# Kernel tuning notes

Measured on AMD Instinct MI355X. Metric: run time of the kernel, lower is better.

## Reference

```python
import jax, jax.numpy as jnp
import numpy as np
import math

B, S, D, H = 8, 1024, 128, 8  # batch, seq, input_dim(=head_dim), head_num

def setup_inputs() -> dict:
    key = jax.random.key(0)
    ks = jax.random.split(key, 12)
    HD = H * D
    sc_in = 1.0 / math.sqrt(D)
    sc_hd = 1.0 / math.sqrt(HD)
    return {
        "query": jax.random.normal(ks[0], (B, S, D), jnp.float32),
        "key":   jax.random.normal(ks[1], (B, S, D), jnp.float32),
        "value": jax.random.normal(ks[2], (B, S, D), jnp.float32),
        "pos":   jax.random.normal(ks[3], (B, S, D), jnp.float32),
        "mask":  jnp.ones((B, S), jnp.int32),
        # torch Linear weights stored as [in, out] for x @ W + b
        "Wq": jax.random.normal(ks[4], (D, HD), jnp.float32) * sc_in,
        "bq": jnp.zeros((HD,), jnp.float32),
        "Wk": jax.random.normal(ks[5], (D, HD), jnp.float32) * sc_in,
        "bk": jnp.zeros((HD,), jnp.float32),
        "Wv": jax.random.normal(ks[6], (D, HD), jnp.float32) * sc_in,
        "bv": jnp.zeros((HD,), jnp.float32),
        "Wo": jax.random.normal(ks[7], (HD, D), jnp.float32) * sc_hd,
        "bo": jnp.zeros((D,), jnp.float32),
    }

def reference(query, key, value, pos, mask, Wq, bq, Wk, bk, Wv, bv, Wo, bo):
    # QKV projections (pos added to all three inputs)
    q = (query + pos) @ Wq + bq  # [B,S,H*D]
    k = (key + pos) @ Wk + bk
    v = (value + pos) @ Wv + bv
    # split heads -> [B,H,S,D]
    q = q.reshape(B, S, H, D).transpose(0, 2, 1, 3)
    k = k.reshape(B, S, H, D).transpose(0, 2, 1, 3)
    v = v.reshape(B, S, H, D).transpose(0, 2, 1, 3)
    scale = 1.0 / math.sqrt(D)
    scores = jnp.einsum("bhqd,bhkd->bhqk", q, k) * scale  # [B,H,S,S]
    # mask [B,S] -> broadcast over heads and query positions
    m = mask[:, None, None, :]  # [B,1,1,S]
    scores = jnp.where(m == 0, jnp.float32(-jnp.inf), scores)
    attn = jax.nn.softmax(scores, axis=-1)  # dropout is identity in eval mode
    out = jnp.einsum("bhqk,bhkd->bhqd", attn, v)
    out = out.transpose(0, 2, 1, 3).reshape(B, S, H * D)
    return out @ Wo + bo  # [B,S,D]
```

## Files before the change

### kernel.cpp

```cpp
#include <hip/hip_runtime.h>
#include <stdint.h>


typedef __attribute__((ext_vector_type(8))) short bf16x8;
typedef __attribute__((ext_vector_type(4))) float f32x4;
typedef unsigned int uint;
typedef unsigned short ushort;

__device__ __forceinline__ float bf2f(short s) {
    return __uint_as_float(((uint)(ushort)s) << 16);
}
__device__ __forceinline__ short f2bf(float f) {
    uint u = __float_as_uint(f);
    u += 0x7fffu + ((u >> 16) & 1u);
    return (short)(u >> 16);
}
__device__ __forceinline__ short f2bf_fast(float f) {
    return (short)((__float_as_uint(f) + 0x8000u) >> 16);
}

__device__ __forceinline__ void dma16(const short* g, short* l) {
    __builtin_amdgcn_global_load_lds(
        (const __attribute__((address_space(1))) uint*)g,
        (__attribute__((address_space(3))) uint*)l, 16, 0, 0);
}

__global__ __launch_bounds__(256) void fill_sentinel(float* __restrict__ out, int n) {
    int i = blockIdx.x * 256 + threadIdx.x;
    if (i < n) out[i] = 128.0f;
}

__global__ __launch_bounds__(256) void transpose_w(
    const float* __restrict__ Wq, const float* __restrict__ Wk,
    const float* __restrict__ Wv, const float* __restrict__ Wo,
    short* __restrict__ WTq, short* __restrict__ WTk,
    short* __restrict__ WTv, short* __restrict__ WoT)
{
    int z = blockIdx.y;
    const float* src; short* dst; int K, N;
    if (z < 3) { K = 128; N = 1024; src = (z==0)?Wq:(z==1)?Wk:Wv; dst = (z==0)?WTq:(z==1)?WTk:WTv; }
    else       { K = 1024; N = 128; src = Wo; dst = WoT; }
    int ntn = N >> 6;
    int nt = blockIdx.x % ntn, kt = blockIdx.x / ntn;
    int k0 = kt * 64, n0 = nt * 64;

    __shared__ __align__(16) short TT[64][72];
    int t = threadIdx.x;
    int r = t >> 2, c4 = t & 3;
    const float4* s4 = (const float4*)&src[(k0 + r) * N + n0 + c4 * 16];
    short* tr = &TT[r][c4 * 16];
#pragma unroll
    for (int i = 0; i < 4; ++i) {
        float4 v = s4[i];
        tr[i * 4 + 0] = f2bf(v.x);
        tr[i * 4 + 1] = f2bf(v.y);
        tr[i * 4 + 2] = f2bf(v.z);
        tr[i * 4 + 3] = f2bf(v.w);
    }
    __syncthreads();
    union { short s[16]; uint4 v[2]; } pk;
#pragma unroll
    for (int i = 0; i < 16; ++i) pk.s[i] = TT[c4 * 16 + i][r];
    uint4* dp = (uint4*)&dst[(n0 + r) * K + k0 + c4 * 16];
    dp[0] = pk.v[0]; dp[1] = pk.v[1];
}

__global__ __launch_bounds__(256) void qkv_proj(
    const float* __restrict__ query, const float* __restrict__ key_,
    const float* __restrict__ value, const float* __restrict__ pos,
    const short* __restrict__ WTq, const short* __restrict__ WTk, const short* __restrict__ WTv,
    const float* __restrict__ bq, const float* __restrict__ bk, const float* __restrict__ bv,
    short* __restrict__ Qg, short* __restrict__ Kg, short* __restrict__ Vtg)
{
    int z = blockIdx.y;
    const float* X    = (z==0) ? query : (z==1) ? key_ : value;
    const short* WT   = (z==0) ? WTq   : (z==1) ? WTk  : WTv;
    const float* bias = (z==0) ? bq    : (z==1) ? bk   : bv;

    __shared__ __align__(16) short Xs[64][136];
    __shared__ __align__(16) short Ws[16 * 512];
    __shared__ __align__(16) short T[64][72];

    int t = threadIdx.x;
    int m0 = blockIdx.x * 64;
    int lane = t & 63, w = t >> 6;
    int l = lane & 15, q = lane >> 4;

    {
        int r = t >> 2, c4 = t & 3;
        const float4* xs = (const float4*)&X[(m0 + r) * 128 + c4 * 32];
        const float4* ps = (const float4*)&pos[(m0 + r) * 128 + c4 * 32];
#pragma unroll
        for (int i = 0; i < 8; ++i) {
            float4 a = xs[i], bb = ps[i];
            uint2 o;
            o.x = (uint)(ushort)f2bf(a.x + bb.x) | ((uint)(ushort)f2bf(a.y + bb.y) << 16);
            o.y = (uint)(ushort)f2bf(a.z + bb.z) | ((uint)(ushort)f2bf(a.w + bb.w) << 16);
            *(uint2*)&Xs[r][c4 * 32 + i * 4] = o;
        }
    }
    __syncthreads();

    bf16x8 aX[4];
#pragma unroll
    for (int k32 = 0; k32 < 4; ++k32)
        aX[k32] = *(const bf16x8*)&Xs[w * 16 + l][k32 * 32 + q * 8];

    int b = m0 >> 10, s0 = m0 & 1023;

    for (int nt = 0; nt < 16; ++nt) {
        int n0 = nt * 64;
        __syncthreads();
        {
            const short* wsrc = &WT[(n0 + w * 16 + l) * 128 + q * 8];
#pragma unroll
            for (int k32 = 0; k32 < 4; ++k32)
                dma16(wsrc + k32 * 32, &Ws[(w * 4 + k32) * 512]);
        }
        __syncthreads();

        f32x4 acc[4];
#pragma unroll
        for (int nb = 0; nb < 4; ++nb) {
            f32x4 c = {0.f, 0.f, 0.f, 0.f};
            const short* wf = &Ws[nb * 2048 + lane * 8];
#pragma unroll
            for (int k32 = 0; k32 < 4; ++k32)
                c = __builtin_amdgcn_mfma_f32_16x16x32_bf16(aX[k32], *(const bf16x8*)(wf + k32 * 512), c, 0, 0, 0);
            acc[nb] = c;
        }

        if (z < 2) {
#pragma unroll
            for (int nb = 0; nb < 4; ++nb) {
                float bi = bias[n0 + nb * 16 + l];
#pragma unroll
                for (int r = 0; r < 4; ++r)
                    T[w * 16 + q * 4 + r][nb * 16 + l] = f2bf(acc[nb][r] + bi);
            }
            __syncthreads();
            short* dst = (z == 0) ? Qg : Kg;
            int row = t >> 2, c16 = t & 3;
            int n = n0 + c16 * 16, h = n >> 7, d0 = n & 127;
            uint4 v0 = *(uint4*)&T[row][c16 * 16];
            uint4 v1 = *(uint4*)&T[row][c16 * 16 + 8];
            uint4* dp = (uint4*)&dst[(((b * 8 + h) * 1024 + s0 + row) << 7) + d0];
            dp[0] = v0; dp[1] = v1;
        } else {
#pragma unroll
            for (int nb = 0; nb < 4; ++nb) {
                float bi = bias[n0 + nb * 16 + l];
#pragma unroll
                for (int r = 0; r < 4; ++r)
                    T[nb * 16 + l][w * 16 + q * 4 + r] = f2bf(acc[nb][r] + bi);
            }
            __syncthreads();
            int nl = t >> 2, mc = t & 3;
            int n = n0 + nl, h = n >> 7, d = n & 127;
            uint4 v0 = *(uint4*)&T[nl][mc * 16];
            uint4 v1 = *(uint4*)&T[nl][mc * 16 + 8];
            uint4* dp = (uint4*)&Vtg[(((b * 8 + h) * 128 + d) << 10) + s0 + mc * 16];
            dp[0] = v0; dp[1] = v1;
        }
    }
}

__global__ __launch_bounds__(256) void attention(
    const short* __restrict__ Qg, const short* __restrict__ Kg,
    const short* __restrict__ Vtg, const int* __restrict__ mask,
    short* __restrict__ AO)
{
    int bh = blockIdx.x & 63;
    int qt = blockIdx.x >> 6;
    int b = bh >> 3, h = bh & 7;
    int q0 = qt << 6;

    __shared__ __align__(16) short Ks[16 * 512];
    __shared__ __align__(16) short Vs[16 * 512];
    __shared__ __align__(16) short Ps[4][16][72];
    __shared__ int Ms[64];

    int t = threadIdx.x, lane = t & 63, w = t >> 6;
    int l = lane & 15, q = lane >> 4;

    bf16x8 aQ[4];
    {
        const short* qp = &Qg[((bh * 1024 + q0 + w * 16 + l) << 7) + q * 8];
#pragma unroll
        for (int k32 = 0; k32 < 4; ++k32)
            aQ[k32] = *(const bf16x8*)(qp + k32 * 32);
    }

    f32x4 O[8];
#pragma unroll
    for (int i = 0; i < 8; ++i) O[i] = {0.f, 0.f, 0.f, 0.f};
    float lrow[4] = {0.f, 0.f, 0.f, 0.f};

    const float SL2E = 0.12752298917458827f;
    const float MAXB = 44.0f;

    const short* kbase = &Kg[((bh * 1024 + w * 16 + l) << 7) + q * 8];
    const short* vb0 = &Vtg[((bh * 128 + (2 * w) * 16 + l) << 10) + q * 8];
    const short* vb1 = &Vtg[((bh * 128 + (2 * w + 1) * 16 + l) << 10) + q * 8];

    for (int kt = 0; kt < 16; ++kt) {
        int k0 = kt << 6;
        __syncthreads();
        {
            const short* kp = kbase + (k0 << 7);
            dma16(kp,      &Ks[(w * 4 + 0) * 512]);
            dma16(kp + 32, &Ks[(w * 4 + 1) * 512]);
            dma16(kp + 64, &Ks[(w * 4 + 2) * 512]);
            dma16(kp + 96, &Ks[(w * 4 + 3) * 512]);
            dma16(vb0 + k0,      &Vs[(4 * w + 0) * 512]);
            dma16(vb0 + k0 + 32, &Vs[(4 * w + 1) * 512]);
            dma16(vb1 + k0,      &Vs[(4 * w + 2) * 512]);
            dma16(vb1 + k0 + 32, &Vs[(4 * w + 3) * 512]);
            if (t < 64) Ms[t] = mask[b * 1024 + k0 + t];
        }
        __syncthreads();

        int mk0 = Ms[l], mk1 = Ms[16 + l], mk2 = Ms[32 + l], mk3 = Ms[48 + l];
        bool allm = (__ballot(mk0 && mk1 && mk2 && mk3) == ~0ull);

        float p[4][4];
#pragma unroll
        for (int nb = 0; nb < 4; ++nb) {
            f32x4 c = {0.f, 0.f, 0.f, 0.f};
            const short* kf = &Ks[nb * 2048 + lane * 8];
#pragma unroll
            for (int k32 = 0; k32 < 4; ++k32)
                c = __builtin_amdgcn_mfma_f32_16x16x32_bf16(aQ[k32], *(const bf16x8*)(kf + k32 * 512), c, 0, 0, 0);
#pragma unroll
            for (int r = 0; r < 4; ++r)
                p[nb][r] = exp2f(fmaf(c[r], SL2E, -MAXB));
        }
        if (!allm) {
            int mks[4] = {mk0, mk1, mk2, mk3};
#pragma unroll
            for (int nb = 0; nb < 4; ++nb)
                if (!mks[nb])
#pragma unroll
                    for (int r = 0; r < 4; ++r) p[nb][r] = 0.f;
        }
#pragma unroll
        for (int nb = 0; nb < 4; ++nb)
#pragma unroll
            for (int r = 0; r < 4; ++r) {
                lrow[r] += p[nb][r];
                Ps[w][q * 4 + r][nb * 16 + l] = f2bf_fast(p[nb][r]);
            }

        bf16x8 aP0 = *(const bf16x8*)&Ps[w][l][q * 8];
        bf16x8 aP1 = *(const bf16x8*)&Ps[w][l][32 + q * 8];
#pragma unroll
        for (int dt = 0; dt < 8; ++dt) {
            f32x4 c = O[dt];
            c = __builtin_amdgcn_mfma_f32_16x16x32_bf16(aP0, *(const bf16x8*)&Vs[(dt * 2 + 0) * 512 + lane * 8], c, 0, 0, 0);
            c = __builtin_amdgcn_mfma_f32_16x16x32_bf16(aP1, *(const bf16x8*)&Vs[(dt * 2 + 1) * 512 + lane * 8], c, 0, 0, 0);
            O[dt] = c;
        }
    }

#pragma unroll
    for (int off = 1; off <= 8; off <<= 1)
#pragma unroll
        for (int r = 0; r < 4; ++r)
            lrow[r] += __shfl_xor(lrow[r], off);
    float rl[4];
#pragma unroll
    for (int r = 0; r < 4; ++r) rl[r] = 1.0f / lrow[r];
#pragma unroll
    for (int dt = 0; dt < 8; ++dt) {
        int col = h * 128 + dt * 16 + l;
#pragma unroll
        for (int r = 0; r < 4; ++r) {
            int s = q0 + w * 16 + q * 4 + r;
            AO[((b * 1024 + s) << 10) + col] = f2bf(O[dt][r] * rl[r]);
        }
    }
}

__global__ __launch_bounds__(256) void out_proj(
    const short* __restrict__ AO, const short* __restrict__ WoT,
    const float* __restrict__ bo, float* __restrict__ out)
{
    __shared__ __align__(16) short As[32][72];
    __shared__ __align__(16) short Bs[16 * 512];

    int t = threadIdx.x, lane = t & 63, w = t >> 6;
    int l = lane & 15, q = lane >> 4;
    int m0 = blockIdx.x * 32;
    int rowh = (w & 1) * 16;
    int nbg = (w >> 1) * 4;

    f32x4 acc[4];
#pragma unroll
    for (int i = 0; i < 4; ++i) acc[i] = {0.f, 0.f, 0.f, 0.f};

    for (int kc = 0; kc < 16; ++kc) {
        int k0 = kc * 64;
        __syncthreads();
        {
            int r = t >> 3, c8 = t & 7;
            *(uint4*)&As[r][c8 * 8] = *(const uint4*)&AO[((m0 + r) << 10) + k0 + c8 * 8];
#pragma unroll
            for (int j = 0; j < 4; ++j) {
                int nb = w * 2 + (j >> 1), k32 = j & 1;
                dma16(&WoT[(nb * 16 + l) * 1024 + k0 + k32 * 32 + q * 8],
                      &Bs[(nb * 2 + k32) * 512]);
            }
        }
        __syncthreads();

        bf16x8 aA0 = *(const bf16x8*)&As[rowh + l][q * 8];
        bf16x8 aA1 = *(const bf16x8*)&As[rowh + l][32 + q * 8];
#pragma unroll
        for (int nb = 0; nb < 4; ++nb) {
            f32x4 c = acc[nb];
            c = __builtin_amdgcn_mfma_f32_16x16x32_bf16(aA0, *(const bf16x8*)&Bs[((nbg + nb) * 2 + 0) * 512 + lane * 8], c, 0, 0, 0);
            c = __builtin_amdgcn_mfma_f32_16x16x32_bf16(aA1, *(const bf16x8*)&Bs[((nbg + nb) * 2 + 1) * 512 + lane * 8], c, 0, 0, 0);
            acc[nb] = c;
        }
    }

#pragma unroll
    for (int nb = 0; nb < 4; ++nb) {
        int n = (nbg + nb) * 16 + l;
        float bi = bo[n];
#pragma unroll
        for (int r = 0; r < 4; ++r) {
            int m = m0 + rowh + q * 4 + r;
            out[(m << 7) + n] = acc[nb][r] + bi;
        }
    }
}

extern "C" void kernel_launch(void* const* d_in, const int* in_sizes, int n_in,
                              void* d_out, int out_size, void* d_ws, size_t ws_size,
                              hipStream_t stream)
{
    const size_t NEED = (size_t)65 * 1024 * 1024;
    if (ws_size < NEED) {
        hipLaunchKernelGGL(fill_sentinel, dim3((out_size + 255) / 256), dim3(256), 0, stream,
                           (float*)d_out, out_size);
        return;
    }

    const float* query = (const float*)d_in[0];
    const float* key_  = (const float*)d_in[1];
    const float* value = (const float*)d_in[2];
    const float* pos   = (const float*)d_in[3];
    const int*   mask  = (const int*)d_in[4];
    const float* Wq = (const float*)d_in[5];
    const float* bq = (const float*)d_in[6];
    const float* Wk = (const float*)d_in[7];
    const float* bk = (const float*)d_in[8];
    const float* Wv = (const float*)d_in[9];
    const float* bv = (const float*)d_in[10];
    const float* Wo = (const float*)d_in[11];
    const float* bo = (const float*)d_in[12];

    char* ws = (char*)d_ws;
    short* Qg  = (short*)(ws);
    short* Kg  = (short*)(ws + (size_t)16 * 1024 * 1024);
    short* Vtg = (short*)(ws + (size_t)32 * 1024 * 1024);
    short* AO  = (short*)(ws + (size_t)48 * 1024 * 1024);
    short* WTq = (short*)(ws + (size_t)64 * 1024 * 1024);
    short* WTk = WTq + 131072;
    short* WTv = WTk + 131072;
    short* WoT = WTv + 131072;

    hipLaunchKernelGGL(transpose_w, dim3(32, 4), dim3(256), 0, stream,
                       Wq, Wk, Wv, Wo, WTq, WTk, WTv, WoT);
    hipLaunchKernelGGL(qkv_proj, dim3(128, 3), dim3(256), 0, stream,
                       query, key_, value, pos, WTq, WTk, WTv, bq, bk, bv, Qg, Kg, Vtg);
    hipLaunchKernelGGL(attention, dim3(1024), dim3(256), 0, stream,
                       Qg, Kg, Vtg, mask, AO);
    hipLaunchKernelGGL(out_proj, dim3(256), dim3(256), 0, stream,
                       AO, WoT, bo, (float*)d_out);
}
```

Before: 223.2 us.

## Double-buffer LDS tiles in QKV, attention and output projection kernels

Converts the weight, K/V and output-projection tile staging from single-buffered to double-buffered LDS. The next tile is prefetched with global_load_lds while the current one feeds the MFMAs, and one of the two barriers per iteration is removed. The attention kernel also loads the whole 1024-entry mask row into LDS once instead of per tile. The cost is roughly twice the LDS footprint per block, which can cut occupancy, and correctness relies on the barrier waiting for outstanding LDS DMA.

```diff
diff --git a/kernel.cpp b/kernel.cpp
--- a/kernel.cpp
+++ b/kernel.cpp
@@ -78,14 +78,20 @@
     const float* bias = (z==0) ? bq    : (z==1) ? bk   : bv;
 
     __shared__ __align__(16) short Xs[64][136];
-    __shared__ __align__(16) short Ws[16 * 512];
-    __shared__ __align__(16) short T[64][72];
+    __shared__ __align__(16) short Ws[2][8192];
+    __shared__ __align__(16) short T[2][64][72];
 
     int t = threadIdx.x;
     int m0 = blockIdx.x * 64;
     int lane = t & 63, w = t >> 6;
     int l = lane & 15, q = lane >> 4;
 
+    const short* wbase = &WT[(w * 16 + l) * 128 + q * 8];
+    {
+#pragma unroll
+        for (int k32 = 0; k32 < 4; ++k32)
+            dma16(wbase + k32 * 32, &Ws[0][(w * 4 + k32) * 512]);
+    }
     {
         int r = t >> 2, c4 = t & 3;
         const float4* xs = (const float4*)&X[(m0 + r) * 128 + c4 * 32];
@@ -109,41 +115,40 @@
     int b = m0 >> 10, s0 = m0 & 1023;
 
     for (int nt = 0; nt < 16; ++nt) {
-        int n0 = nt * 64;
-        __syncthreads();
-        {
-            const short* wsrc = &WT[(n0 + w * 16 + l) * 128 + q * 8];
+        int cur = nt & 1;
+        if (nt < 15) {
+            const short* wsrc = wbase + (nt + 1) * 64 * 128;
 #pragma unroll
             for (int k32 = 0; k32 < 4; ++k32)
-                dma16(wsrc + k32 * 32, &Ws[(w * 4 + k32) * 512]);
-        }
-        __syncthreads();
+                dma16(wsrc + k32 * 32, &Ws[cur ^ 1][(w * 4 + k32) * 512]);
+        }
 
         f32x4 acc[4];
 #pragma unroll
         for (int nb = 0; nb < 4; ++nb) {
             f32x4 c = {0.f, 0.f, 0.f, 0.f};
-            const short* wf = &Ws[nb * 2048 + lane * 8];
+            const short* wf = &Ws[cur][nb * 2048 + lane * 8];
 #pragma unroll
             for (int k32 = 0; k32 < 4; ++k32)
                 c = __builtin_amdgcn_mfma_f32_16x16x32_bf16(aX[k32], *(const bf16x8*)(wf + k32 * 512), c, 0, 0, 0);
             acc[nb] = c;
         }
 
+        int n0 = nt * 64;
         if (z < 2) {
 #pragma unroll
             for (int nb = 0; nb < 4; ++nb) {
                 float bi = bias[n0 + nb * 16 + l];
 #pragma unroll
                 for (int r = 0; r < 4; ++r)
-                    T[w * 16 + q * 4 + r][nb * 16 + l] = f2bf(acc[nb][r] + bi);
+                    T[cur][w * 16 + q * 4 + r][nb * 16 + l] = f2bf(acc[nb][r] + bi);
             }
             __syncthreads();
             short* dst = (z == 0) ? Qg : Kg;
             int row = t >> 2, c16 = t & 3;
             int n = n0 + c16 * 16, h = n >> 7, d0 = n & 127;
-            uint4 v0 = *(uint4*)&T[row][c16 * 16];
-            uint4 v1 = *(uint4*)&T[row][c16 * 16 + 8];
+            uint4 v0 = *(uint4*)&T[cur][row][c16 * 16];
+            uint4 v1 = *(uint4*)&T[cur][row][c16 * 16 + 8];
             uint4* dp = (uint4*)&dst[(((b * 8 + h) * 1024 + s0 + row) << 7) + d0];
             dp[0] = v0; dp[1] = v1;
         } else {
@@ -152,13 +157,13 @@
                 float bi = bias[n0 + nb * 16 + l];
 #pragma unroll
                 for (int r = 0; r < 4; ++r)
-                    T[nb * 16 + l][w * 16 + q * 4 + r] = f2bf(acc[nb][r] + bi);
+                    T[cur][nb * 16 + l][w * 16 + q * 4 + r] = f2bf(acc[nb][r] + bi);
             }
             __syncthreads();
             int nl = t >> 2, mc = t & 3;
             int n = n0 + nl, h = n >> 7, d = n & 127;
-            uint4 v0 = *(uint4*)&T[nl][mc * 16];
-            uint4 v1 = *(uint4*)&T[nl][mc * 16 + 8];
+            uint4 v0 = *(uint4*)&T[cur][nl][mc * 16];
+            uint4 v1 = *(uint4*)&T[cur][nl][mc * 16 + 8];
             uint4* dp = (uint4*)&Vtg[(((b * 8 + h) * 128 + d) << 10) + s0 + mc * 16];
             dp[0] = v0; dp[1] = v1;
         }
@@ -175,13 +180,15 @@
     int b = bh >> 3, h = bh & 7;
     int q0 = qt << 6;
 
-    __shared__ __align__(16) short Ks[16 * 512];
-    __shared__ __align__(16) short Vs[16 * 512];
+    __shared__ __align__(16) short Ks[2][8192];
+    __shared__ __align__(16) short Vs[2][8192];
     __shared__ __align__(16) short Ps[4][16][72];
-    __shared__ int Ms[64];
+    __shared__ int Ms[1024];
 
     int t = threadIdx.x, lane = t & 63, w = t >> 6;
     int l = lane & 15, q = lane >> 4;
+
+    *(int4*)&Ms[t * 4] = *(const int4*)&mask[b * 1024 + t * 4];
 
     bf16x8 aQ[4];
     {
@@ -191,43 +198,54 @@
             aQ[k32] = *(const bf16x8*)(qp + k32 * 32);
     }
 
-    f32x4 O[8];
-#pragma unroll
-    for (int i = 0; i < 8; ++i) O[i] = {0.f, 0.f, 0.f, 0.f};
-    float lrow[4] = {0.f, 0.f, 0.f, 0.f};
-
-    const float SL2E = 0.12752298917458827f;
-    const float MAXB = 44.0f;
-
     const short* kbase = &Kg[((bh * 1024 + w * 16 + l) << 7) + q * 8];
     const short* vb0 = &Vtg[((bh * 128 + (2 * w) * 16 + l) << 10) + q * 8];
     const short* vb1 = &Vtg[((bh * 128 + (2 * w + 1) * 16 + l) << 10) + q * 8];
 
+    {
+        dma16(kbase,      &Ks[0][(w * 4 + 0) * 512]);
+        dma16(kbase + 32, &Ks[0][(w * 4 + 1) * 512]);
+        dma16(kbase + 64, &Ks[0][(w * 4 + 2) * 512]);
+        dma16(kbase + 96, &Ks[0][(w * 4 + 3) * 512]);
+        dma16(vb0,      &Vs[0][(4 * w + 0) * 512]);
+        dma16(vb0 + 32, &Vs[0][(4 * w + 1) * 512]);
+        dma16(vb1,      &Vs[0][(4 * w + 2) * 512]);
+        dma16(vb1 + 32, &Vs[0][(4 * w + 3) * 512]);
+    }
+
+    f32x4 O[8];
+#pragma unroll
+    for (int i = 0; i < 8; ++i) O[i] = {0.f, 0.f, 0.f, 0.f};
+    float lrow[4] = {0.f, 0.f, 0.f, 0.f};
+
+    const float SL2E = 0.12752298917458827f;
+    const float MAXB = 44.0f;
+
     for (int kt = 0; kt < 16; ++kt) {
+        __syncthreads();
+        int cur = kt & 1;
+        if (kt < 15) {
+            int k1 = (kt + 1) << 6;
+            const short* kp = kbase + (k1 << 7);
+            dma16(kp,      &Ks[cur ^ 1][(w * 4 + 0) * 512]);
+            dma16(kp + 32, &Ks[cur ^ 1][(w * 4 + 1) * 512]);
+            dma16(kp + 64, &Ks[cur ^ 1][(w * 4 + 2) * 512]);
+            dma16(kp + 96, &Ks[cur ^ 1][(w * 4 + 3) * 512]);
+            dma16(vb0 + k1,      &Vs[cur ^ 1][(4 * w + 0) * 512]);
+            dma16(vb0 + k1 + 32, &Vs[cur ^ 1][(4 * w + 1) * 512]);
+            dma16(vb1 + k1,      &Vs[cur ^ 1][(4 * w + 2) * 512]);
+            dma16(vb1 + k1 + 32, &Vs[cur ^ 1][(4 * w + 3) * 512]);
+        }
+
         int k0 = kt << 6;
-        __syncthreads();
-        {
-            const short* kp = kbase + (k0 << 7);
-            dma16(kp,      &Ks[(w * 4 + 0) * 512]);
-            dma16(kp + 32, &Ks[(w * 4 + 1) * 512]);
-            dma16(kp + 64, &Ks[(w * 4 + 2) * 512]);
-            dma16(kp + 96, &Ks[(w * 4 + 3) * 512]);
-            dma16(vb0 + k0,      &Vs[(4 * w + 0) * 512]);
-            dma16(vb0 + k0 + 32, &Vs[(4 * w + 1) * 512]);
-            dma16(vb1 + k0,      &Vs[(4 * w + 2) * 512]);
-            dma16(vb1 + k0 + 32, &Vs[(4 * w + 3) * 512]);
-            if (t < 64) Ms[t] = mask[b * 1024 + k0 + t];
-        }
-        __syncthreads();
-
-        int mk0 = Ms[l], mk1 = Ms[16 + l], mk2 = Ms[32 + l], mk3 = Ms[48 + l];
+        int mk0 = Ms[k0 + l], mk1 = Ms[k0 + 16 + l], mk2 = Ms[k0 + 32 + l], mk3 = Ms[k0 + 48 + l];
         bool allm = (__ballot(mk0 && mk1 && mk2 && mk3) == ~0ull);
 
         float p[4][4];
 #pragma unroll
         for (int nb = 0; nb < 4; ++nb) {
             f32x4 c = {0.f, 0.f, 0.f, 0.f};
-            const short* kf = &Ks[nb * 2048 + lane * 8];
+            const short* kf = &Ks[cur][nb * 2048 + lane * 8];
 #pragma unroll
             for (int k32 = 0; k32 < 4; ++k32)
                 c = __builtin_amdgcn_mfma_f32_16x16x32_bf16(aQ[k32], *(const bf16x8*)(kf + k32 * 512), c, 0, 0, 0);
@@ -256,8 +274,8 @@
 #pragma unroll
         for (int dt = 0; dt < 8; ++dt) {
             f32x4 c = O[dt];
-            c = __builtin_amdgcn_mfma_f32_16x16x32_bf16(aP0, *(const bf16x8*)&Vs[(dt * 2 + 0) * 512 + lane * 8], c, 0, 0, 0);
-            c = __builtin_amdgcn_mfma_f32_16x16x32_bf16(aP1, *(const bf16x8*)&Vs[(dt * 2 + 1) * 512 + lane * 8], c, 0, 0, 0);
+            c = __builtin_amdgcn_mfma_f32_16x16x32_bf16(aP0, *(const bf16x8*)&Vs[cur][(dt * 2 + 0) * 512 + lane * 8], c, 0, 0, 0);
+            c = __builtin_amdgcn_mfma_f32_16x16x32_bf16(aP1, *(const bf16x8*)&Vs[cur][(dt * 2 + 1) * 512 + lane * 8], c, 0, 0, 0);
             O[dt] = c;
         }
     }
@@ -285,8 +303,8 @@
     const short* __restrict__ AO, const short* __restrict__ WoT,
     const float* __restrict__ bo, float* __restrict__ out)
 {
-    __shared__ __align__(16) short As[32][72];
-    __shared__ __align__(16) short Bs[16 * 512];
+    __shared__ __align__(16) short As[2][32][72];
+    __shared__ __align__(16) short Bs[2][8192];
 
     int t = threadIdx.x, lane = t & 63, w = t >> 6;
     int l = lane & 15, q = lane >> 4;
@@ -294,34 +312,47 @@
     int rowh = (w & 1) * 16;
     int nbg = (w >> 1) * 4;
 
+    int ar = t >> 3, ac8 = t & 7;
+    {
+        *(uint4*)&As[0][ar][ac8 * 8] = *(const uint4*)&AO[((m0 + ar) << 10) + ac8 * 8];
+#pragma unroll
+        for (int j = 0; j < 4; ++j) {
+            int nb = w * 2 + (j >> 1), k32 = j & 1;
+            dma16(&WoT[(nb * 16 + l) * 1024 + k32 * 32 + q * 8], &Bs[0][(nb * 2 + k32) * 512]);
+        }
+    }
+
     f32x4 acc[4];
 #pragma unroll
     for (int i = 0; i < 4; ++i) acc[i] = {0.f, 0.f, 0.f, 0.f};
 
     for (int kc = 0; kc < 16; ++kc) {
-        int k0 = kc * 64;
         __syncthreads();
-        {
-            int r = t >> 3, c8 = t & 7;
-            *(uint4*)&As[r][c8 * 8] = *(const uint4*)&AO[((m0 + r) << 10) + k0 + c8 * 8];
+        int cur = kc & 1;
+        uint4 anext;
+        if (kc < 15) {
+            int k1 = (kc + 1) * 64;
+            anext = *(const uint4*)&AO[((m0 + ar) << 10) + k1 + ac8 * 8];
 #pragma unroll
             for (int j = 0; j < 4; ++j) {
                 int nb = w * 2 + (j >> 1), k32 = j & 1;
-                dma16(&WoT[(nb * 16 + l) * 1024 + k0 + k32 * 32 + q * 8],
-                      &Bs[(nb * 2 + k32) * 512]);
+                dma16(&WoT[(nb * 16 + l) * 1024 + k1 + k32 * 32 + q * 8],
+                      &Bs[cur ^ 1][(nb * 2 + k32) * 512]);
             }
         }
-        __syncthreads();
-
-        bf16x8 aA0 = *(const bf16x8*)&As[rowh + l][q * 8];
-        bf16x8 aA1 = *(const bf16x8*)&As[rowh + l][32 + q * 8];
+
+        bf16x8 aA0 = *(const bf16x8*)&As[cur][rowh + l][q * 8];
+        bf16x8 aA1 = *(const bf16x8*)&As[cur][rowh + l][32 + q * 8];
 #pragma unroll
         for (int nb = 0; nb < 4; ++nb) {
             f32x4 c = acc[nb];
-            c = __builtin_amdgcn_mfma_f32_16x16x32_bf16(aA0, *(const bf16x8*)&Bs[((nbg + nb) * 2 + 0) * 512 + lane * 8], c, 0, 0, 0);
-            c = __builtin_amdgcn_mfma_f32_16x16x32_bf16(aA1, *(const bf16x8*)&Bs[((nbg + nb) * 2 + 1) * 512 + lane * 8], c, 0, 0, 0);
+            c = __builtin_amdgcn_mfma_f32_16x16x32_bf16(aA0, *(const bf16x8*)&Bs[cur][((nbg + nb) * 2 + 0) * 512 + lane * 8], c, 0, 0, 0);
+            c = __builtin_amdgcn_mfma_f32_16x16x32_bf16(aA1, *(const bf16x8*)&Bs[cur][((nbg + nb) * 2 + 1) * 512 + lane * 8], c, 0, 0, 0);
             acc[nb] = c;
         }
+
+        if (kc < 15)
+            *(uint4*)&As[cur ^ 1][ar][ac8 * 8] = anext;
     }
 
 #pragma unroll
```

Measured after the change: 221.6 us. No clear change (-0.7%).
